# Optimization experiments

Measured on AMD Instinct MI355X. Metric: run time of the kernel, lower is better.

The kernel has to match this reference:

```python
import jax, jax.numpy as jnp
import numpy as np

THRESHOLD = 8.0
B, C, H, W = 16, 512, 56, 56


def setup_inputs() -> dict:
    key = jax.random.key(0)
    # scale by 3 so per-channel max|x| ~ 13 > threshold -> channels disassemble with T=2
    x = jax.random.normal(key, (B, C, H, W), dtype=jnp.float32) * 3.0
    return {"x": x}


def _plan(x):
    """Host-side plan (mirrors the .item() host sync in the torch module).
    Returns outlier channel ids, the gather index that replicates each outlier
    channel T times, and the matching 1/T scale per output channel."""
    xv = np.asarray(x)
    max_vals = np.max(np.abs(xv), axis=(0, 2, 3))              # [C] per-channel max|x|
    outlier_idx = np.nonzero(max_vals > THRESHOLD)[0]          # channels to disassemble
    T = np.ceil(max_vals[outlier_idx] / THRESHOLD).astype(np.int64)
    rep_idx = np.repeat(outlier_idx, T)                        # each outlier channel repeated T times
    inv_T = np.repeat((1.0 / T).astype(np.float32), T)         # per-output-channel scale 1/T
    return outlier_idx, rep_idx, inv_T


def reference(x):
    outlier_idx, rep_idx, inv_T = _plan(x)
    rep = jnp.asarray(rep_idx)
    scale = jnp.asarray(inv_T)
    # single fused gather + scale replaces the per-channel slice/divide/repeat/concat loop
    disassembled_x = x[:, rep, :, :] * scale[None, :, None, None]
    return disassembled_x, jnp.asarray(outlier_idx)
```

## Files before the change

### kernel.cpp

```cpp
#include <hip/hip_runtime.h>

#define CH    512
#define BATCH 16
#define HW    3136
#define HW4   784
#define THRESH 8.0f

typedef float f4 __attribute__((ext_vector_type(4)));

__global__ __launch_bounds__(256) void absmax_kernel(const float* __restrict__ x,
                                                     float* __restrict__ partial) {
    const int c   = blockIdx.x;
    const int b   = blockIdx.y;
    const int tid = threadIdx.x;
    const f4* src = reinterpret_cast<const f4*>(x) + (size_t)(b * CH + c) * HW4;
    float m = 0.0f;
    for (int p = tid; p < HW4; p += 256) {
        f4 v = src[p];
        m = fmaxf(m, fmaxf(fmaxf(fabsf(v.x), fabsf(v.y)),
                           fmaxf(fabsf(v.z), fabsf(v.w))));
    }
    __shared__ float sm[256];
    sm[tid] = m;
    __syncthreads();
    for (int off = 128; off > 0; off >>= 1) {
        if (tid < off) sm[tid] = fmaxf(sm[tid], sm[tid + off]);
        __syncthreads();
    }
    if (tid == 0) partial[c * BATCH + b] = sm[0];
}

__global__ __launch_bounds__(CH) void plan_kernel(const float* __restrict__ partial,
                                                  int*   __restrict__ rep,
                                                  float* __restrict__ invT,
                                                  float* __restrict__ out_tail) {
    const int t = threadIdx.x;
    float m = 0.0f;
    #pragma unroll
    for (int k = 0; k < BATCH; ++k) m = fmaxf(m, partial[t * BATCH + k]);

    int T = 0;
    if (m > THRESH) T = (int)ceilf(m * 0.125f);
    int isout = (T > 0) ? 1 : 0;

    __shared__ int sT[CH];
    __shared__ int sO[CH];
    sT[t] = T;
    sO[t] = isout;
    __syncthreads();
    for (int off = 1; off < CH; off <<= 1) {
        int a = 0, bb = 0;
        if (t >= off) { a = sT[t - off]; bb = sO[t - off]; }
        __syncthreads();
        sT[t] += a;
        sO[t] += bb;
        __syncthreads();
    }
    if (T > 0) {
        int s = sT[t] - T;
        int o = sO[t] - isout;
        out_tail[o] = (float)t;
        float iv = (float)(1.0 / (double)T);
        for (int k = 0; k < T; ++k) {
            rep[s + k]  = t;
            invT[s + k] = iv;
        }
    }
}

__global__ __launch_bounds__(256) void gather_kernel(const float* __restrict__ x,
                                                     const int*   __restrict__ rep,
                                                     const float* __restrict__ invT,
                                                     float* __restrict__ out,
                                                     int R) {
    const int nwg  = gridDim.x;
    const int orig = blockIdx.x;
    const int xcd  = orig & 7;
    const int q = nwg >> 3, r = nwg & 7;
    const int wg = (xcd < r ? xcd * (q + 1) : r * (q + 1) + (xcd - r) * q)
                   + (orig >> 3);
    const int j = wg >> 4;
    const int b = wg & 15;

    const int   c = rep[j];
    const float s = invT[j];
    const f4* src = reinterpret_cast<const f4*>(x) + (size_t)(b * CH + c) * HW4;
    f4* dst = reinterpret_cast<f4*>(out) + ((size_t)b * R + j) * HW4;
    for (int p = threadIdx.x; p < HW4; p += 256) {
        f4 v = src[p];
        v.x *= s; v.y *= s; v.z *= s; v.w *= s;
        __builtin_nontemporal_store(v, &dst[p]);
    }
}

extern "C" void kernel_launch(void* const* d_in, const int* in_sizes, int n_in,
                              void* d_out, int out_size, void* d_ws, size_t ws_size,
                              hipStream_t stream) {
    const float* x = (const float*)d_in[0];
    float* out = (float*)d_out;

    const int plane = BATCH * HW;
    const int R     = out_size / plane;
    const int n_out = out_size - R * plane;
    (void)n_out;

    float* partial = (float*)d_ws;
    int*   rep  = (int*)  ((char*)d_ws + (size_t)CH * BATCH * 4);
    float* invT = (float*)((char*)d_ws + (size_t)CH * BATCH * 4 + (size_t)R * 4);

    absmax_kernel<<<dim3(CH, BATCH), 256, 0, stream>>>(x, partial);
    plan_kernel<<<1, CH, 0, stream>>>(partial, rep, invT, out + (size_t)R * plane);
    if (R > 0) {
        gather_kernel<<<dim3(R * BATCH), 256, 0, stream>>>(x, rep, invT, out, R);
    }
}
```

Before: 71.12 us.

## Fuse plan computation into gather kernel and coarsen absmax over batch groups

Drops the single-block plan kernel. Every gather workgroup now recomputes the per-channel T values from the partial maxima with a wave-shuffle prefix scan, then finds its own source channel and scale. The absmax kernel now reduces 4 batches per block, so the partial buffer shrinks to 4 entries per channel, which fit one float4 read. This removes one kernel launch and a serialized one-block step, but makes every gather block do redundant scan work and adds extra syncthreads.

Result: faster. 66.62 us (-6.3%).

```diff
diff --git a/kernel.cpp b/kernel.cpp
--- a/kernel.cpp
+++ b/kernel.cpp
@@ -2,6 +2,8 @@
 
 #define CH    512
 #define BATCH 16
+#define QB    4
+#define NQ    (BATCH / QB)
 #define HW    3136
 #define HW4   784
 #define THRESH 8.0f
@@ -11,14 +13,17 @@
 __global__ __launch_bounds__(256) void absmax_kernel(const float* __restrict__ x,
                                                      float* __restrict__ partial) {
     const int c   = blockIdx.x;
-    const int b   = blockIdx.y;
+    const int q   = blockIdx.y;
     const int tid = threadIdx.x;
-    const f4* src = reinterpret_cast<const f4*>(x) + (size_t)(b * CH + c) * HW4;
     float m = 0.0f;
-    for (int p = tid; p < HW4; p += 256) {
-        f4 v = src[p];
-        m = fmaxf(m, fmaxf(fmaxf(fabsf(v.x), fabsf(v.y)),
-                           fmaxf(fabsf(v.z), fabsf(v.w))));
+    for (int bb = 0; bb < QB; ++bb) {
+        const int b = q * QB + bb;
+        const f4* src = reinterpret_cast<const f4*>(x) + (size_t)(b * CH + c) * HW4;
+        for (int p = tid; p < HW4; p += 256) {
+            f4 v = src[p];
+            m = fmaxf(m, fmaxf(fmaxf(fabsf(v.x), fabsf(v.y)),
+                               fmaxf(fabsf(v.z), fabsf(v.w))));
+        }
     }
     __shared__ float sm[256];
     sm[tid] = m;
@@ -27,69 +32,85 @@
         if (tid < off) sm[tid] = fmaxf(sm[tid], sm[tid + off]);
         __syncthreads();
     }
-    if (tid == 0) partial[c * BATCH + b] = sm[0];
-}
-
-__global__ __launch_bounds__(CH) void plan_kernel(const float* __restrict__ partial,
-                                                  int*   __restrict__ rep,
-                                                  float* __restrict__ invT,
-                                                  float* __restrict__ out_tail) {
-    const int t = threadIdx.x;
-    float m = 0.0f;
-    #pragma unroll
-    for (int k = 0; k < BATCH; ++k) m = fmaxf(m, partial[t * BATCH + k]);
-
-    int T = 0;
-    if (m > THRESH) T = (int)ceilf(m * 0.125f);
-    int isout = (T > 0) ? 1 : 0;
-
-    __shared__ int sT[CH];
-    __shared__ int sO[CH];
-    sT[t] = T;
-    sO[t] = isout;
-    __syncthreads();
-    for (int off = 1; off < CH; off <<= 1) {
-        int a = 0, bb = 0;
-        if (t >= off) { a = sT[t - off]; bb = sO[t - off]; }
-        __syncthreads();
-        sT[t] += a;
-        sO[t] += bb;
-        __syncthreads();
-    }
-    if (T > 0) {
-        int s = sT[t] - T;
-        int o = sO[t] - isout;
-        out_tail[o] = (float)t;
-        float iv = (float)(1.0 / (double)T);
-        for (int k = 0; k < T; ++k) {
-            rep[s + k]  = t;
-            invT[s + k] = iv;
-        }
-    }
+    if (tid == 0) partial[c * NQ + q] = sm[0];
 }
 
 __global__ __launch_bounds__(256) void gather_kernel(const float* __restrict__ x,
-                                                     const int*   __restrict__ rep,
-                                                     const float* __restrict__ invT,
+                                                     const float* __restrict__ partial,
                                                      float* __restrict__ out,
+                                                     float* __restrict__ out_tail,
                                                      int R) {
     const int nwg  = gridDim.x;
     const int orig = blockIdx.x;
     const int xcd  = orig & 7;
-    const int q = nwg >> 3, r = nwg & 7;
-    const int wg = (xcd < r ? xcd * (q + 1) : r * (q + 1) + (xcd - r) * q)
+    const int q8 = nwg >> 3, r8 = nwg & 7;
+    const int wg = (xcd < r8 ? xcd * (q8 + 1) : r8 * (q8 + 1) + (xcd - r8) * q8)
                    + (orig >> 3);
     const int j = wg >> 4;
     const int b = wg & 15;
 
-    const int   c = rep[j];
-    const float s = invT[j];
+    const int tid  = threadIdx.x;
+    const int lane = tid & 63;
+    const int w    = tid >> 6;
+
+    const int c0 = tid * 2, c1 = c0 + 1;
+    f4 p0 = reinterpret_cast<const f4*>(partial)[tid * 2];
+    f4 p1 = reinterpret_cast<const f4*>(partial)[tid * 2 + 1];
+    float m0 = fmaxf(fmaxf(p0.x, p0.y), fmaxf(p0.z, p0.w));
+    float m1 = fmaxf(fmaxf(p1.x, p1.y), fmaxf(p1.z, p1.w));
+    int T0 = (m0 > THRESH) ? (int)ceilf(m0 * 0.125f) : 0;
+    int T1 = (m1 > THRESH) ? (int)ceilf(m1 * 0.125f) : 0;
+    const int v = T0 + T1;
+
+    int s = v;
+    #pragma unroll
+    for (int off = 1; off < 64; off <<= 1) {
+        int t2 = __shfl_up(s, off, 64);
+        if (lane >= off) s += t2;
+    }
+    __shared__ int wsum[4];
+    if (lane == 63) wsum[w] = s;
+    __syncthreads();
+    int woff = 0;
+    #pragma unroll
+    for (int k = 0; k < 4; ++k) if (k < w) woff += wsum[k];
+    const int excl   = woff + s - v;
+    const int start0 = excl, start1 = excl + T0;
+
+    __shared__ int sc, sT;
+    if (T0 > 0 && j >= start0 && j < start0 + T0) { sc = c0; sT = T0; }
+    if (T1 > 0 && j >= start1 && j < start1 + T1) { sc = c1; sT = T1; }
+
+    if (wg == 0) {
+        const int o0 = (T0 > 0), o1 = (T1 > 0);
+        const int v2 = o0 + o1;
+        int s2 = v2;
+        #pragma unroll
+        for (int off = 1; off < 64; off <<= 1) {
+            int t2 = __shfl_up(s2, off, 64);
+            if (lane >= off) s2 += t2;
+        }
+        __shared__ int wsum2[4];
+        if (lane == 63) wsum2[w] = s2;
+        __syncthreads();
+        int woff2 = 0;
+        #pragma unroll
+        for (int k = 0; k < 4; ++k) if (k < w) woff2 += wsum2[k];
+        const int ex2 = woff2 + s2 - v2;
+        if (o0) out_tail[ex2]      = (float)c0;
+        if (o1) out_tail[ex2 + o0] = (float)c1;
+    }
+    __syncthreads();
+
+    const int   c     = sc;
+    const float scale = (float)(1.0 / (double)sT);
+
     const f4* src = reinterpret_cast<const f4*>(x) + (size_t)(b * CH + c) * HW4;
     f4* dst = reinterpret_cast<f4*>(out) + ((size_t)b * R + j) * HW4;
-    for (int p = threadIdx.x; p < HW4; p += 256) {
-        f4 v = src[p];
-        v.x *= s; v.y *= s; v.z *= s; v.w *= s;
-        __builtin_nontemporal_store(v, &dst[p]);
+    for (int p = tid; p < HW4; p += 256) {
+        f4 vv = src[p];
+        vv.x *= scale; vv.y *= scale; vv.z *= scale; vv.w *= scale;
+        __builtin_nontemporal_store(vv, &dst[p]);
     }
 }
 
@@ -101,16 +122,12 @@
 
     const int plane = BATCH * HW;
     const int R     = out_size / plane;
-    const int n_out = out_size - R * plane;
-    (void)n_out;
 
     float* partial = (float*)d_ws;
-    int*   rep  = (int*)  ((char*)d_ws + (size_t)CH * BATCH * 4);
-    float* invT = (float*)((char*)d_ws + (size_t)CH * BATCH * 4 + (size_t)R * 4);
 
-    absmax_kernel<<<dim3(CH, BATCH), 256, 0, stream>>>(x, partial);
-    plan_kernel<<<1, CH, 0, stream>>>(partial, rep, invT, out + (size_t)R * plane);
+    absmax_kernel<<<dim3(CH, NQ), 256, 0, stream>>>(x, partial);
     if (R > 0) {
-        gather_kernel<<<dim3(R * BATCH), 256, 0, stream>>>(x, rep, invT, out, R);
+        gather_kernel<<<dim3(R * BATCH), 256, 0, stream>>>(
+            x, partial, out, out + (size_t)R * plane, R);
     }
 }
```
